# Kernel tuning notes

Hardware: AMD Instinct MI355X
Metric: run time of the kernel (lower is better)

Reference implementation:

```python
import jax, jax.numpy as jnp
import numpy as np

D = 2048       # hidden / input / output width
DEPTH = 9      # infinite_depth (layer default)


def _infinite_layer(x, inf_w, cls_w, cls_b):
    """Faithful vectorized InfiniteNeuralLayer.forward.

    Original per-(sample, j, depth) Python loops build a circulant rotation
    matrix M = cos*I + sin*(shift_down - shift_up) and apply it 3x per depth
    with angles inf_w[depth, j, 0..2]. The rotated state never depends on x,
    so we carry one state row per output index j and scan over the 27 angle
    steps, expressing M @ s as cos*s + sin*(roll(s,1) - roll(s,-1)).
    infinite_biases is unused in the original forward and is omitted.
    """
    dim = x.shape[1]
    classical = x @ cls_w + cls_b                      # [B, dim]
    # angles per j per depth step: (DEPTH, dim_j, 3) -> sequence (DEPTH*3, dim_j)
    angles = jnp.transpose(inf_w[:, :, :3], (0, 2, 1)).reshape(-1, dim)
    init = jnp.full((dim, dim), 1.0 / np.sqrt(dim), dtype=x.dtype)  # [j, state]

    def step(s, a):
        c = jnp.cos(a)[:, None]
        sn = jnp.sin(a)[:, None]
        s_new = c * s + sn * (jnp.roll(s, 1, axis=1) - jnp.roll(s, -1, axis=1))
        return s_new, None

    state, _ = jax.lax.scan(step, init, angles)        # [dim_j, dim]
    p = state[:, 0] ** 2                               # |state[0]|^2 per j
    return jnp.tanh(classical + p[None, :])            # broadcast over batch


def setup_inputs() -> dict:
    key = jax.random.key(0)
    ks = jax.random.split(key, 16)
    s = 0.02  # keep activations in sane range (original uses raw randn)
    f = jax.random.normal
    return {
        "x":      f(ks[0], (2048, D), dtype=jnp.float32),
        "w0":     f(ks[1], (D, D), dtype=jnp.float32) * s,
        "b0":     f(ks[2], (D,), dtype=jnp.float32) * s,
        "w1":     f(ks[3], (D, D), dtype=jnp.float32) * s,
        "b1":     f(ks[4], (D,), dtype=jnp.float32) * s,
        "inf_w1": f(ks[5], (DEPTH, D, D), dtype=jnp.float32),
        "cls_w1": f(ks[6], (D, D), dtype=jnp.float32) * s,
        "cls_b1": f(ks[7], (D,), dtype=jnp.float32) * s,
        "w2":     f(ks[8], (D, D), dtype=jnp.float32) * s,
        "b2":     f(ks[9], (D,), dtype=jnp.float32) * s,
        "inf_w2": f(ks[10], (DEPTH, D, D), dtype=jnp.float32),
        "cls_w2": f(ks[11], (D, D), dtype=jnp.float32) * s,
        "cls_b2": f(ks[12], (D,), dtype=jnp.float32) * s,
        "w3":     f(ks[13], (D, D), dtype=jnp.float32) * s,
        "b3":     f(ks[14], (D,), dtype=jnp.float32) * s,
    }


def reference(x, w0, b0, w1, b1, inf_w1, cls_w1, cls_b1,
              w2, b2, inf_w2, cls_w2, cls_b2, w3, b3):
    h = jax.nn.relu(x @ w0 + b0)
    h = jax.nn.relu(h @ w1 + b1)
    h = _infinite_layer(h, inf_w1, cls_w1, cls_b1)
    h = jax.nn.relu(h @ w2 + b2)
    h = _infinite_layer(h, inf_w2, cls_w2, cls_b2)
    return jax.nn.relu(h @ w3 + b3)
```

## Files before the change

### kernel.cpp

```cpp
#include <hip/hip_runtime.h>
#include <hip/hip_bf16.h>


#define DD 2048
#define DEPTH 9

#define BM 128
#define BN 64
#define BK 32
#define NT (DD / BK)
#define ABUF (BM * BK)
#define BBUF (BN * BK)
#define NBUF 6

typedef __attribute__((ext_vector_type(8))) short short8;
typedef __attribute__((ext_vector_type(4))) float f32x4;

__device__ __forceinline__ unsigned short f2bf(float f) {
  unsigned u = __float_as_uint(f);
  u += 0x7FFFu + ((u >> 16) & 1u);
  return (unsigned short)(u >> 16);
}

__global__ __launch_bounds__(256) void prep_kernel(
    const float* __restrict__ w0, const float* __restrict__ w1,
    unsigned short* __restrict__ wts, const float* __restrict__ x,
    unsigned short* __restrict__ xb, const float* __restrict__ infw1,
    const float* __restrict__ infw2, const float* __restrict__ clsb1,
    const float* __restrict__ clsb2, float* __restrict__ padd1,
    float* __restrict__ padd2) {
  int b = blockIdx.x;
  int tid = threadIdx.x;
  if (b < 8192) {
    __shared__ float tile[32][33];
    int z = b >> 12;
    int t = b & 4095;
    const float* src = z ? w1 : w0;
    unsigned short* dst = wts + (size_t)z * DD * DD;
    int bx = (t & 63) * 32;
    int by = (t >> 6) * 32;
    int tx = tid & 31, ty = tid >> 5;
#pragma unroll
    for (int i = ty; i < 32; i += 8)
      tile[i][tx] = src[(size_t)(by + i) * DD + bx + tx];
    __syncthreads();
#pragma unroll
    for (int i = ty; i < 32; i += 8)
      dst[(size_t)(bx + i) * DD + by + tx] = f2bf(tile[tx][i]);
  } else if (b < 12288) {
    int i = (b - 8192) * 256 + tid;
    float4 v = reinterpret_cast<const float4*>(x)[i];
    ushort4 o;
    o.x = f2bf(v.x); o.y = f2bf(v.y); o.z = f2bf(v.z); o.w = f2bf(v.w);
    reinterpret_cast<ushort4*>(xb)[i] = o;
  } else {
    int jj = (b - 12288) * 256 + tid;
    int layer = jj >> 11;
    int j = jj & 2047;
    const float* inf_w = layer ? infw2 : infw1;
    const float* cls_b = layer ? clsb2 : clsb1;
    float* padd = layer ? padd2 : padd1;
    float prod = 1.0f;
#pragma unroll
    for (int d = 0; d < DEPTH; ++d) {
      const float* row = inf_w + ((size_t)d * DD + j) * DD;
      prod *= cosf(row[0]) * cosf(row[1]) * cosf(row[2]);
    }
    padd[j] = cls_b[j] + prod * prod * (1.0f / (float)DD);
  }
}


__device__ __forceinline__ void gload_lds16(const unsigned short* g,
                                            unsigned short* l) {
  __builtin_amdgcn_global_load_lds(
      (const __attribute__((address_space(1))) void*)g,
      (__attribute__((address_space(3))) void*)l, 16, 0, 0);
}

template <int EPI>
__global__ __launch_bounds__(256) void gemm_kernel(
    const unsigned short* __restrict__ A, const unsigned short* __restrict__ Bt,
    const float* __restrict__ bias, unsigned short* __restrict__ Cb,
    float* __restrict__ Cf, const float* __restrict__ tsrc,
    unsigned short* __restrict__ tdst) {
  const int N = DD, K = DD;
  __shared__ __align__(16) unsigned char smem[73728];
  unsigned short* As = (unsigned short*)smem;
  unsigned short* Bs = (unsigned short*)(smem + NBUF * ABUF * 2);

  int tid = threadIdx.x;
  int wid = tid >> 6, lane = tid & 63;
  int wr = wid >> 1, wc = wid & 1;
  int lr = lane & 15;
  int lg = lane >> 4;

  int bid = blockIdx.x;
  int swz = (bid & 7) * 64 + (bid >> 3);
  int bcol = (swz & 31) * BN;
  int brow = (swz >> 5) * BM;

  const unsigned short* Abase = A + (size_t)brow * K;
  const unsigned short* Bbase = Bt + (size_t)bcol * K;

  auto stage = [&](int buf, int tile) {
    int kt = tile * BK;
#pragma unroll
    for (int r = 0; r < 2; ++r) {
      int chunk = r * 256 + tid;
      int row = chunk >> 2;
      int sp = chunk & 3;
      int kof = (sp ^ ((row >> 1) & 3)) * 8;
      gload_lds16(Abase + (size_t)row * K + kt + kof,
                  As + buf * ABUF + (size_t)(r * 256 + wid * 64) * 8);
    }
    {
      int row = tid >> 2;
      int sp = tid & 3;
      int kof = (sp ^ ((row >> 1) & 3)) * 8;
      gload_lds16(Bbase + (size_t)row * K + kt + kof,
                  Bs + buf * BBUF + (size_t)(wid * 64) * 8);
    }
  };

  f32x4 acc[4][2];
#pragma unroll
  for (int i = 0; i < 4; ++i)
#pragma unroll
    for (int j = 0; j < 2; ++j) acc[i][j] = f32x4{0.f, 0.f, 0.f, 0.f};

  auto compute = [&](int buf) {
    short8 a[4], b[2];
#pragma unroll
    for (int mt = 0; mt < 4; ++mt) {
      int row = wr * 64 + mt * 16 + lr;
      int slot = lg ^ ((row >> 1) & 3);
      a[mt] = *reinterpret_cast<const short8*>(
          &As[buf * ABUF + row * BK + slot * 8]);
    }
#pragma unroll
    for (int nt = 0; nt < 2; ++nt) {
      int row = wc * 32 + nt * 16 + lr;
      int slot = lg ^ ((row >> 1) & 3);
      b[nt] = *reinterpret_cast<const short8*>(
          &Bs[buf * BBUF + row * BK + slot * 8]);
    }
    __builtin_amdgcn_s_setprio(1);
#pragma unroll
    for (int mt = 0; mt < 4; ++mt)
#pragma unroll
      for (int nt = 0; nt < 2; ++nt)
        acc[mt][nt] = __builtin_amdgcn_mfma_f32_16x16x32_bf16(
            a[mt], b[nt], acc[mt][nt], 0, 0, 0);
    __builtin_amdgcn_s_setprio(0);
  };

  auto step = [&](int buf, int pf_tile, int wcase) {
    if (wcase == 0) asm volatile("s_waitcnt vmcnt(12)" ::: "memory");
    else if (wcase == 1) asm volatile("s_waitcnt vmcnt(9)" ::: "memory");
    else if (wcase == 2) asm volatile("s_waitcnt vmcnt(6)" ::: "memory");
    else if (wcase == 3) asm volatile("s_waitcnt vmcnt(3)" ::: "memory");
    else asm volatile("s_waitcnt vmcnt(0)" ::: "memory");
    __builtin_amdgcn_s_barrier();
    __builtin_amdgcn_sched_barrier(0);
    compute(buf);
    if (pf_tile < NT) stage(pf_tile % NBUF, pf_tile);
  };

  stage(0, 0); stage(1, 1); stage(2, 2); stage(3, 3); stage(4, 4);
#pragma unroll 1
  for (int i = 0; i < 10; ++i) {
    int t = 6 * i;
    step(0, t + 5, 0);
    step(1, t + 6, 0);
    step(2, t + 7, 0);
    step(3, t + 8, 0);
    step(4, t + 9, 0);
    step(5, t + 10, 0);
  }
  step(0, NT, 1);
  step(1, NT, 2);
  step(2, NT, 3);
  step(3, NT, 4);

  {
    float* et = reinterpret_cast<float*>(smem);
    __syncthreads();
#pragma unroll
    for (int nt = 0; nt < 2; ++nt) {
      int colb = wc * 32 + nt * 16 + lr;
      float bs = bias[bcol + colb];
#pragma unroll
      for (int mt = 0; mt < 4; ++mt) {
#pragma unroll
        for (int i = 0; i < 4; ++i) {
          int rowb = wr * 64 + mt * 16 + lg * 4 + i;
          float v = acc[mt][nt][i] + bs;
          v = (EPI == 1) ? tanhf(v) : fmaxf(v, 0.0f);
          et[rowb * 68 + colb] = v;
        }
      }
    }
    __syncthreads();
#pragma unroll
    for (int it = 0; it < 4; ++it) {
      int chunk = it * 256 + tid;
      int rowb = chunk >> 3;
      int c8 = (chunk & 7) * 8;
      float4 v0 = *reinterpret_cast<const float4*>(&et[rowb * 68 + c8]);
      float4 v1 = *reinterpret_cast<const float4*>(&et[rowb * 68 + c8 + 4]);
      size_t g = (size_t)(brow + rowb) * N + bcol + c8;
      if (EPI == 2) {
        *reinterpret_cast<float4*>(&Cf[g]) = v0;
        *reinterpret_cast<float4*>(&Cf[g + 4]) = v1;
      } else {
        uint4 o;
        o.x = (unsigned)f2bf(v0.x) | ((unsigned)f2bf(v0.y) << 16);
        o.y = (unsigned)f2bf(v0.z) | ((unsigned)f2bf(v0.w) << 16);
        o.z = (unsigned)f2bf(v1.x) | ((unsigned)f2bf(v1.y) << 16);
        o.w = (unsigned)f2bf(v1.z) | ((unsigned)f2bf(v1.w) << 16);
        *reinterpret_cast<uint4*>(&Cb[g]) = o;
      }
    }
  }

  if (tsrc != nullptr) {
    float* ft = reinterpret_cast<float*>(smem);
    __syncthreads();
#pragma unroll 1
    for (int t2 = 0; t2 < 2; ++t2) {
      int tau = bid * 2 + t2;
      int bx = (tau & 31) * 64;
      int by = (tau >> 5) * 64;
      if (t2) __syncthreads();
#pragma unroll
      for (int it = 0; it < 4; ++it) {
        int idx = it * 256 + tid;
        int r = idx >> 4, c4 = (idx & 15) * 4;
        float4 v = *reinterpret_cast<const float4*>(
            &tsrc[(size_t)(by + r) * DD + bx + c4]);
        ft[r * 65 + c4 + 0] = v.x;
        ft[r * 65 + c4 + 1] = v.y;
        ft[r * 65 + c4 + 2] = v.z;
        ft[r * 65 + c4 + 3] = v.w;
      }
      __syncthreads();
#pragma unroll
      for (int it = 0; it < 4; ++it) {
        int idx = it * 256 + tid;
        int n = idx >> 4, kq = idx & 15;
        ushort4 o;
        o.x = f2bf(ft[(kq * 4 + 0) * 65 + n]);
        o.y = f2bf(ft[(kq * 4 + 1) * 65 + n]);
        o.z = f2bf(ft[(kq * 4 + 2) * 65 + n]);
        o.w = f2bf(ft[(kq * 4 + 3) * 65 + n]);
        *reinterpret_cast<ushort4*>(&tdst[(size_t)(bx + n) * DD + by + kq * 4]) = o;
      }
    }
  }
}


extern "C" void kernel_launch(void* const* d_in, const int* in_sizes, int n_in,
                              void* d_out, int out_size, void* d_ws,
                              size_t ws_size, hipStream_t stream) {
  const float* x     = (const float*)d_in[0];
  const float* w0    = (const float*)d_in[1];
  const float* b0    = (const float*)d_in[2];
  const float* w1    = (const float*)d_in[3];
  const float* b1    = (const float*)d_in[4];
  const float* infw1 = (const float*)d_in[5];
  const float* clsw1 = (const float*)d_in[6];
  const float* clsb1 = (const float*)d_in[7];
  const float* w2    = (const float*)d_in[8];
  const float* b2    = (const float*)d_in[9];
  const float* infw2 = (const float*)d_in[10];
  const float* clsw2 = (const float*)d_in[11];
  const float* clsb2 = (const float*)d_in[12];
  const float* w3    = (const float*)d_in[13];
  const float* b3    = (const float*)d_in[14];
  float* out = (float*)d_out;

  char* ws = (char*)d_ws;
  const size_t MB = 1ull << 20;
  const size_t DDe = (size_t)DD * DD;
  unsigned short* buf0 = (unsigned short*)ws;
  unsigned short* buf1 = (unsigned short*)(ws + 8 * MB);
  unsigned short* wts  = (unsigned short*)(ws + 16 * MB);
  float* padd1 = (float*)(ws + 64 * MB);
  float* padd2 = padd1 + DD;

  prep_kernel<<<12304, 256, 0, stream>>>(w0, w1, wts, x, buf0, infw1, infw2,
                                         clsb1, clsb2, padd1, padd2);

  dim3 gg((DD / BM) * (DD / BN));
  gemm_kernel<0><<<gg, 256, 0, stream>>>(buf0, wts + 0 * DDe, b0,    buf1,
                                         nullptr, clsw1, wts + 2 * DDe);
  gemm_kernel<0><<<gg, 256, 0, stream>>>(buf1, wts + 1 * DDe, b1,    buf0,
                                         nullptr, w2,    wts + 3 * DDe);
  gemm_kernel<1><<<gg, 256, 0, stream>>>(buf0, wts + 2 * DDe, padd1, buf1,
                                         nullptr, clsw2, wts + 4 * DDe);
  gemm_kernel<0><<<gg, 256, 0, stream>>>(buf1, wts + 3 * DDe, b2,    buf0,
                                         nullptr, w3,    wts + 5 * DDe);
  gemm_kernel<1><<<gg, 256, 0, stream>>>(buf0, wts + 4 * DDe, padd2, buf1,
                                         nullptr, nullptr, nullptr);
  gemm_kernel<2><<<gg, 256, 0, stream>>>(buf1, wts + 5 * DDe, b3,    nullptr,
                                         out, nullptr, nullptr);
}
```

Measured before the change: 222.0 us.

## Double GEMM K-tile to 64 with triple-buffered LDS pipeline and extra barrier

Raises the K tile from 32 to 64 and replaces the six-deep LDS ring with three buffers, adjusting the XOR swizzle to eight slots and splitting compute into two k-substeps. The aim is fewer barrier and waitcnt rounds per unit of MFMA work. A second barrier after each compute guards buffer reuse and adds some synchronization cost, and the shallower prefetch depth may expose more global-load latency.

After: 184.6 us. 16.9% less time.

```diff
diff --git a/kernel.cpp b/kernel.cpp
--- a/kernel.cpp
+++ b/kernel.cpp
@@ -7,11 +7,10 @@
 
 #define BM 128
 #define BN 64
-#define BK 32
+#define BK 64
 #define NT (DD / BK)
 #define ABUF (BM * BK)
 #define BBUF (BN * BK)
-#define NBUF 6
 
 typedef __attribute__((ext_vector_type(8))) short short8;
 typedef __attribute__((ext_vector_type(4))) float f32x4;
@@ -87,7 +86,7 @@
   const int N = DD, K = DD;
   __shared__ __align__(16) unsigned char smem[73728];
   unsigned short* As = (unsigned short*)smem;
-  unsigned short* Bs = (unsigned short*)(smem + NBUF * ABUF * 2);
+  unsigned short* Bs = (unsigned short*)(smem + 3 * ABUF * 2);
 
   int tid = threadIdx.x;
   int wid = tid >> 6, lane = tid & 63;
@@ -106,20 +105,22 @@
   auto stage = [&](int buf, int tile) {
     int kt = tile * BK;
 #pragma unroll
+    for (int r = 0; r < 4; ++r) {
+      int chunk = r * 256 + tid;
+      int row = chunk >> 3;
+      int sp = chunk & 7;
+      int kof = (sp ^ ((row >> 1) & 7)) * 8;
+      gload_lds16(Abase + (size_t)row * K + kt + kof,
+                  As + buf * ABUF + (size_t)(r * 256 + wid * 64) * 8);
+    }
+#pragma unroll
     for (int r = 0; r < 2; ++r) {
       int chunk = r * 256 + tid;
-      int row = chunk >> 2;
-      int sp = chunk & 3;
-      int kof = (sp ^ ((row >> 1) & 3)) * 8;
-      gload_lds16(Abase + (size_t)row * K + kt + kof,
-                  As + buf * ABUF + (size_t)(r * 256 + wid * 64) * 8);
-    }
-    {
-      int row = tid >> 2;
-      int sp = tid & 3;
-      int kof = (sp ^ ((row >> 1) & 3)) * 8;
+      int row = chunk >> 3;
+      int sp = chunk & 7;
+      int kof = (sp ^ ((row >> 1) & 7)) * 8;
       gload_lds16(Bbase + (size_t)row * K + kt + kof,
-                  Bs + buf * BBUF + (size_t)(wid * 64) * 8);
+                  Bs + buf * BBUF + (size_t)(r * 256 + wid * 64) * 8);
     }
   };
 
@@ -130,58 +131,57 @@
     for (int j = 0; j < 2; ++j) acc[i][j] = f32x4{0.f, 0.f, 0.f, 0.f};
 
   auto compute = [&](int buf) {
-    short8 a[4], b[2];
-#pragma unroll
-    for (int mt = 0; mt < 4; ++mt) {
-      int row = wr * 64 + mt * 16 + lr;
-      int slot = lg ^ ((row >> 1) & 3);
-      a[mt] = *reinterpret_cast<const short8*>(
-          &As[buf * ABUF + row * BK + slot * 8]);
-    }
-#pragma unroll
-    for (int nt = 0; nt < 2; ++nt) {
-      int row = wc * 32 + nt * 16 + lr;
-      int slot = lg ^ ((row >> 1) & 3);
-      b[nt] = *reinterpret_cast<const short8*>(
-          &Bs[buf * BBUF + row * BK + slot * 8]);
-    }
-    __builtin_amdgcn_s_setprio(1);
-#pragma unroll
-    for (int mt = 0; mt < 4; ++mt)
-#pragma unroll
-      for (int nt = 0; nt < 2; ++nt)
-        acc[mt][nt] = __builtin_amdgcn_mfma_f32_16x16x32_bf16(
-            a[mt], b[nt], acc[mt][nt], 0, 0, 0);
-    __builtin_amdgcn_s_setprio(0);
+#pragma unroll
+    for (int ks = 0; ks < 2; ++ks) {
+      short8 a[4], b[2];
+#pragma unroll
+      for (int mt = 0; mt < 4; ++mt) {
+        int row = wr * 64 + mt * 16 + lr;
+        int slot = (ks * 4 + lg) ^ ((row >> 1) & 7);
+        a[mt] = *reinterpret_cast<const short8*>(
+            &As[buf * ABUF + row * BK + slot * 8]);
+      }
+#pragma unroll
+      for (int nt = 0; nt < 2; ++nt) {
+        int row = wc * 32 + nt * 16 + lr;
+        int slot = (ks * 4 + lg) ^ ((row >> 1) & 7);
+        b[nt] = *reinterpret_cast<const short8*>(
+            &Bs[buf * BBUF + row * BK + slot * 8]);
+      }
+      __builtin_amdgcn_s_setprio(1);
+#pragma unroll
+      for (int mt = 0; mt < 4; ++mt)
+#pragma unroll
+        for (int nt = 0; nt < 2; ++nt)
+          acc[mt][nt] = __builtin_amdgcn_mfma_f32_16x16x32_bf16(
+              a[mt], b[nt], acc[mt][nt], 0, 0, 0);
+      __builtin_amdgcn_s_setprio(0);
+    }
   };
 
   auto step = [&](int buf, int pf_tile, int wcase) {
     if (wcase == 0) asm volatile("s_waitcnt vmcnt(12)" ::: "memory");
-    else if (wcase == 1) asm volatile("s_waitcnt vmcnt(9)" ::: "memory");
-    else if (wcase == 2) asm volatile("s_waitcnt vmcnt(6)" ::: "memory");
-    else if (wcase == 3) asm volatile("s_waitcnt vmcnt(3)" ::: "memory");
+    else if (wcase == 1) asm volatile("s_waitcnt vmcnt(6)" ::: "memory");
     else asm volatile("s_waitcnt vmcnt(0)" ::: "memory");
     __builtin_amdgcn_s_barrier();
     __builtin_amdgcn_sched_barrier(0);
     compute(buf);
-    if (pf_tile < NT) stage(pf_tile % NBUF, pf_tile);
+    asm volatile("s_waitcnt lgkmcnt(0)" ::: "memory");
+    __builtin_amdgcn_s_barrier();
+    __builtin_amdgcn_sched_barrier(0);
+    if (pf_tile < NT) stage(pf_tile % 3, pf_tile);
   };
 
-  stage(0, 0); stage(1, 1); stage(2, 2); stage(3, 3); stage(4, 4);
+  stage(0, 0); stage(1, 1); stage(2, 2);
 #pragma unroll 1
   for (int i = 0; i < 10; ++i) {
-    int t = 6 * i;
-    step(0, t + 5, 0);
-    step(1, t + 6, 0);
-    step(2, t + 7, 0);
-    step(3, t + 8, 0);
-    step(4, t + 9, 0);
-    step(5, t + 10, 0);
+    int t = 3 * i;
+    step(0, t + 3, 0);
+    step(1, t + 4, 0);
+    step(2, t + 5, 0);
   }
   step(0, NT, 1);
   step(1, NT, 2);
-  step(2, NT, 3);
-  step(3, NT, 4);
 
   {
     float* et = reinterpret_cast<float*>(smem);
```
